# Performance work log

Hardware: AMD Instinct MI355X
Metric: run time of the kernel (lower is better)

Reference implementation:

```python
import jax, jax.numpy as jnp
import numpy as np

SIGMOID_H = np.array([-0.00443981, 0.0244156, -0.01410327, 0.01784681, -0.00239246, 0.06331808, 0.01457577, 0.01753613, 0.01339214, -0.0131252, 0.02026613, 0.00109124, -0.01996419, 0.00723148, 0.03052537, -0.00465259], dtype=np.float32)
SIGMOID_D = np.array([-0.04305673, 2.0701091e-05, -0.028386816, 0.065610707, 0.071529418, -0.0010542608, 0.0012044241, 0.00077212957, -0.00072495628, 0.0010990113, 0.00087419833, -0.0031887756, -0.019837018, 0.00030188679, 0.00022616754, -0.0017746047], dtype=np.float32)
SIGMOID_T = np.array([-0.1190194, 0.03273299, -0.05586114, 0.07758415, -0.06072911, 0.04350465, -0.06501344, -0.07967568, -0.08437239, -0.07040057, -0.07470815, 0.01298669, 0.12695177, 0.00617064, -0.08909994, 0.05016604], dtype=np.float32)


@jax.custom_vjp
def spike(v_scaled):
    # Heaviside with surrogate gradient (triangular) as in SpikeFunction
    return (v_scaled > 0).astype(v_scaled.dtype)

def _spike_fwd(v_scaled):
    return spike(v_scaled), v_scaled

def _spike_bwd(v_scaled, g):
    dz = jnp.maximum(1.0 - jnp.abs(v_scaled), 0.0)
    return (g * dz,)

spike.defvjp(_spike_fwd, _spike_bwd)


def setup_inputs() -> dict:
    key = jax.random.key(0)
    x = jax.random.normal(key, (32, 4096, 1024), dtype=jnp.float32)
    return {
        "x": x,
        "h": jnp.asarray(SIGMOID_H),
        "d": jnp.asarray(SIGMOID_D),
        "T": jnp.asarray(SIGMOID_T),
    }


def reference(x, h, d, T):
    signs = jax.lax.stop_gradient(jnp.sign(x))
    x_abs = jnp.abs(x)
    zeros = jnp.zeros_like(x_abs)

    def step(carry, hdT):
        v, z, out = carry
        ht, dt, Tt = hdT
        v = v - z * ht
        v_scaled = (v - Tt) / (jnp.abs(v) + 1.0)
        z = spike(v_scaled)
        out = out + z * dt
        return (v, z, out), None

    (_, _, out), _ = jax.lax.scan(step, (x_abs, zeros, zeros), (h, d, T))
    return out * signs
```

## Files before the change

kernel.cpp:

```cpp
#include <hip/hip_runtime.h>


typedef float f32x4 __attribute__((ext_vector_type(4)));

__device__ __forceinline__ float spike_elem(float xj, const float* nh,
                                            const float* dd, const float* TT) {
    float v = fabsf(xj);
    float z = 0.0f;
    float o = 0.0f;
#pragma unroll
    for (int t = 0; t < 16; ++t) {
        v = fmaf(z, nh[t], v);
        z = (v > TT[t]) ? 1.0f : 0.0f;
        o = fmaf(z, dd[t], o);
    }
    o = copysignf(o, xj);
    return (xj == 0.0f) ? 0.0f : o;
}

__global__ __launch_bounds__(256) void spike_scan_kernel(
    const float* __restrict__ x,
    const float* __restrict__ h,
    const float* __restrict__ d,
    const float* __restrict__ T,
    float* __restrict__ out,
    long long n4, long long n)
{
    float nh[16], dd[16], TT[16];
#pragma unroll
    for (int t = 0; t < 16; ++t) {
        nh[t] = __int_as_float(__builtin_amdgcn_readfirstlane(__float_as_int(-h[t])));
        dd[t] = __int_as_float(__builtin_amdgcn_readfirstlane(__float_as_int(d[t])));
        TT[t] = __int_as_float(__builtin_amdgcn_readfirstlane(__float_as_int(T[t])));
    }

    const long long i = (long long)blockIdx.x * blockDim.x + threadIdx.x;

    if (i < n4) {
        const f32x4* __restrict__ x4 = reinterpret_cast<const f32x4*>(x);
        f32x4* __restrict__ o4 = reinterpret_cast<f32x4*>(out);
        f32x4 a = x4[i];
        f32x4 r;
#pragma unroll
        for (int j = 0; j < 4; ++j) r[j] = spike_elem(a[j], nh, dd, TT);
        __builtin_nontemporal_store(r, &o4[i]);
    }

    const long long tail_start = n4 * 4;
    if (blockIdx.x == 0) {
        for (long long k = tail_start + threadIdx.x; k < n; k += blockDim.x) {
            out[k] = spike_elem(x[k], nh, dd, TT);
        }
    }
}

extern "C" void kernel_launch(void* const* d_in, const int* in_sizes, int n_in,
                              void* d_out, int out_size, void* d_ws, size_t ws_size,
                              hipStream_t stream) {
    const float* x = (const float*)d_in[0];
    const float* h = (const float*)d_in[1];
    const float* d = (const float*)d_in[2];
    const float* T = (const float*)d_in[3];
    float* out = (float*)d_out;

    const long long n = (long long)out_size;
    const long long n4 = n / 4;

    const int block = 256;
    long long grid_ll = (n4 + block - 1) / block;
    if (grid_ll < 1) grid_ll = 1;
    const int grid = (int)grid_ll;

    spike_scan_kernel<<<grid, block, 0, stream>>>(x, h, d, T, out, n4, n);
}
```

Measured before the change: 235.3 us.

## Process two float4 chunks per thread using packed FP32 FMA

Each thread now loads two float4 vectors, one from each half of the array, and runs the 16-step spike recurrence on them with v_pk_fma_f32 packed FMAs operating on pairs of lanes. The first step is peeled, since z starts at zero and the outcome depends only on T[0]. The grid is halved and launch bounds request two blocks per CU. This targets ALU instruction count and gives more memory parallelism per thread, at the cost of higher register pressure.

```diff
diff --git a/kernel.cpp b/kernel.cpp
--- a/kernel.cpp
+++ b/kernel.cpp
@@ -1,7 +1,14 @@
 #include <hip/hip_runtime.h>
 
 
+typedef float f32x2 __attribute__((ext_vector_type(2)));
 typedef float f32x4 __attribute__((ext_vector_type(4)));
+
+__device__ __forceinline__ f32x2 pk_fma(f32x2 a, f32x2 b, f32x2 c) {
+    f32x2 r;
+    asm("v_pk_fma_f32 %0, %1, %2, %3" : "=v"(r) : "v"(a), "v"(b), "v"(c));
+    return r;
+}
 
 __device__ __forceinline__ float spike_elem(float xj, const float* nh,
                                             const float* dd, const float* TT) {
@@ -18,12 +25,13 @@
     return (xj == 0.0f) ? 0.0f : o;
 }
 
-__global__ __launch_bounds__(256) void spike_scan_kernel(
+__global__ __launch_bounds__(256, 2) void spike_scan_kernel(
     const float* __restrict__ x,
     const float* __restrict__ h,
     const float* __restrict__ d,
     const float* __restrict__ T,
     float* __restrict__ out,
+    long long H,
     long long n4, long long n)
 {
     float nh[16], dd[16], TT[16];
@@ -33,21 +41,66 @@
         dd[t] = __int_as_float(__builtin_amdgcn_readfirstlane(__float_as_int(d[t])));
         TT[t] = __int_as_float(__builtin_amdgcn_readfirstlane(__float_as_int(T[t])));
     }
+    f32x2 nh2[16], dd2[16];
+#pragma unroll
+    for (int t = 1; t < 16; ++t) {
+        f32x2 ca = {nh[t], nh[t]}; asm("" : "+v"(ca)); nh2[t] = ca;
+        f32x2 cb = {dd[t], dd[t]}; asm("" : "+v"(cb)); dd2[t] = cb;
+    }
 
     const long long i = (long long)blockIdx.x * blockDim.x + threadIdx.x;
 
-    if (i < n4) {
+    if (i < H) {
         const f32x4* __restrict__ x4 = reinterpret_cast<const f32x4*>(x);
         f32x4* __restrict__ o4 = reinterpret_cast<f32x4*>(out);
+
         f32x4 a = x4[i];
-        f32x4 r;
+        f32x4 b = x4[i + H];
+
+        f32x2 va = {fabsf(a[0]), fabsf(a[1])};
+        f32x2 vb = {fabsf(a[2]), fabsf(a[3])};
+        f32x2 vc = {fabsf(b[0]), fabsf(b[1])};
+        f32x2 vd = {fabsf(b[2]), fabsf(b[3])};
+        f32x2 za = {1.0f, 1.0f}, zb = {1.0f, 1.0f};
+        f32x2 zc = {1.0f, 1.0f}, zd = {1.0f, 1.0f};
+        f32x2 oa = {dd[0], dd[0]}, ob = {dd[0], dd[0]};
+        f32x2 oc = {dd[0], dd[0]}, od = {dd[0], dd[0]};
+
 #pragma unroll
-        for (int j = 0; j < 4; ++j) r[j] = spike_elem(a[j], nh, dd, TT);
-        __builtin_nontemporal_store(r, &o4[i]);
+        for (int t = 1; t < 16; ++t) {
+            va = pk_fma(za, nh2[t], va);
+            vb = pk_fma(zb, nh2[t], vb);
+            vc = pk_fma(zc, nh2[t], vc);
+            vd = pk_fma(zd, nh2[t], vd);
+            za[0] = (va[0] > TT[t]) ? 1.0f : 0.0f;
+            za[1] = (va[1] > TT[t]) ? 1.0f : 0.0f;
+            zb[0] = (vb[0] > TT[t]) ? 1.0f : 0.0f;
+            zb[1] = (vb[1] > TT[t]) ? 1.0f : 0.0f;
+            zc[0] = (vc[0] > TT[t]) ? 1.0f : 0.0f;
+            zc[1] = (vc[1] > TT[t]) ? 1.0f : 0.0f;
+            zd[0] = (vd[0] > TT[t]) ? 1.0f : 0.0f;
+            zd[1] = (vd[1] > TT[t]) ? 1.0f : 0.0f;
+            oa = pk_fma(za, dd2[t], oa);
+            ob = pk_fma(zb, dd2[t], ob);
+            oc = pk_fma(zc, dd2[t], oc);
+            od = pk_fma(zd, dd2[t], od);
+        }
+
+        f32x4 ra, rb;
+        ra[0] = (a[0] == 0.0f) ? 0.0f : copysignf(oa[0], a[0]);
+        ra[1] = (a[1] == 0.0f) ? 0.0f : copysignf(oa[1], a[1]);
+        ra[2] = (a[2] == 0.0f) ? 0.0f : copysignf(ob[0], a[2]);
+        ra[3] = (a[3] == 0.0f) ? 0.0f : copysignf(ob[1], a[3]);
+        rb[0] = (b[0] == 0.0f) ? 0.0f : copysignf(oc[0], b[0]);
+        rb[1] = (b[1] == 0.0f) ? 0.0f : copysignf(oc[1], b[1]);
+        rb[2] = (b[2] == 0.0f) ? 0.0f : copysignf(od[0], b[2]);
+        rb[3] = (b[3] == 0.0f) ? 0.0f : copysignf(od[1], b[3]);
+        __builtin_nontemporal_store(ra, &o4[i]);
+        __builtin_nontemporal_store(rb, &o4[i + H]);
     }
 
-    const long long tail_start = n4 * 4;
-    if (blockIdx.x == 0) {
+    const long long tail_start = 8 * H;
+    if (blockIdx.x == 0 && tail_start < n) {
         for (long long k = tail_start + threadIdx.x; k < n; k += blockDim.x) {
             out[k] = spike_elem(x[k], nh, dd, TT);
         }
@@ -65,11 +118,12 @@
 
     const long long n = (long long)out_size;
     const long long n4 = n / 4;
+    const long long H = n4 / 2;
 
     const int block = 256;
-    long long grid_ll = (n4 + block - 1) / block;
+    long long grid_ll = (H + block - 1) / block;
     if (grid_ll < 1) grid_ll = 1;
     const int grid = (int)grid_ll;
 
-    spike_scan_kernel<<<grid, block, 0, stream>>>(x, h, d, T, out, n4, n);
+    spike_scan_kernel<<<grid, block, 0, stream>>>(x, h, d, T, out, H, n4, n);
 }
```

Result: no change. 233.9 us (-0.6%).
